# Kernel tuning notes

Hardware: AMD Instinct MI355X
Metric: run time of the kernel (lower is better)

Reference implementation:

```python
import jax, jax.numpy as jnp
import numpy as np

N_HEADS = 32
N_KV_HEADS = 8
HEAD_DIM = 64
ROPE_BASE = 10000.0


def _rope(t):
    # t: [b, s, h, d]; Llama-style rotate-half RoPE
    b, s, h, d = t.shape
    inv_freq = 1.0 / (ROPE_BASE ** (jnp.arange(0, d, 2, dtype=jnp.float32) / d))
    freqs = jnp.arange(s, dtype=jnp.float32)[:, None] * inv_freq[None, :]  # [s, d/2]
    cos = jnp.cos(freqs)[None, :, None, :].astype(t.dtype)
    sin = jnp.sin(freqs)[None, :, None, :].astype(t.dtype)
    t1, t2 = t[..., : d // 2], t[..., d // 2 :]
    return jnp.concatenate([t1 * cos - t2 * sin, t2 * cos + t1 * sin], axis=-1)


def setup_inputs() -> dict:
    key = jax.random.key(0)
    ks = jax.random.split(key, 5)
    b, s, d = 2, 2048, 2048
    dkv = d // (N_HEADS // N_KV_HEADS)
    sc = 1.0 / np.sqrt(d)
    return {
        "x": jax.random.normal(ks[0], (b, s, d), jnp.float32),
        "wq": jax.random.normal(ks[1], (d, d), jnp.float32) * sc,
        "wk": jax.random.normal(ks[2], (d, dkv), jnp.float32) * sc,
        "wv": jax.random.normal(ks[3], (d, dkv), jnp.float32) * sc,
        "wo": jax.random.normal(ks[4], (d, d), jnp.float32) * sc,
    }


def reference(x, wq, wk, wv, wo):
    b, s, d = x.shape
    g = N_HEADS // N_KV_HEADS
    q = (x @ wq).reshape(b, s, N_HEADS, HEAD_DIM)
    k = (x @ wk).reshape(b, s, N_KV_HEADS, HEAD_DIM)
    v = (x @ wv).reshape(b, s, N_KV_HEADS, HEAD_DIM)
    q = _rope(q)
    k = _rope(k)
    # GQA: repeat kv heads to match query heads
    k = jnp.repeat(k, g, axis=2)  # [b, s, N_HEADS, d_h]
    v = jnp.repeat(v, g, axis=2)
    scale = 1.0 / np.sqrt(HEAD_DIM)
    scores = jnp.einsum("bqhd,bkhd->bhqk", q, k) * scale  # [b, h, s, s]
    causal = jnp.tril(jnp.ones((s, s), dtype=bool))
    scores = jnp.where(causal[None, None], scores, jnp.finfo(scores.dtype).min)
    probs = jax.nn.softmax(scores, axis=-1)
    out = jnp.einsum("bhqk,bkhd->bqhd", probs, v).reshape(b, s, d)
    return out @ wo
```

## Files before the change

kernel.cpp:

```cpp
#include <hip/hip_runtime.h>
#include <hip/hip_bf16.h>
#include <stdint.h>

typedef __attribute__((ext_vector_type(8))) __bf16 bf16x8;
typedef __attribute__((ext_vector_type(4))) __bf16 bf16x4;
typedef __attribute__((ext_vector_type(4))) float f32x4;

#define QSCALE (0.125f * 1.44269504f)

#define GL16(src, dst) __builtin_amdgcn_global_load_lds( \
    (const __attribute__((address_space(1))) void*)(src), \
    (__attribute__((address_space(3))) void*)(dst), 16, 0, 0)

static __device__ inline unsigned pkbf(float a, float b) {
  __bf16 x = (__bf16)a, y = (__bf16)b;
  unsigned short ux = __builtin_bit_cast(unsigned short, x);
  unsigned short uy = __builtin_bit_cast(unsigned short, y);
  return ((unsigned)uy << 16) | ux;
}

static __device__ inline float ex2(float x) {
#if __has_builtin(__builtin_amdgcn_exp2f)
  return __builtin_amdgcn_exp2f(x);
#else
  float r;
  asm("v_exp_f32 %0, %1" : "=v"(r) : "v"(x));
  return r;
#endif
}

__global__ void k_cvt(const float* __restrict__ in, __bf16* __restrict__ out, int n8) {
  int i = blockIdx.x * blockDim.x + threadIdx.x;
  if (i >= n8) return;
  const float4* p = (const float4*)(in) + (size_t)i * 2;
  float4 a = p[0], b = p[1];
  bf16x8 o;
  o[0] = (__bf16)a.x; o[1] = (__bf16)a.y; o[2] = (__bf16)a.z; o[3] = (__bf16)a.w;
  o[4] = (__bf16)b.x; o[5] = (__bf16)b.y; o[6] = (__bf16)b.z; o[7] = (__bf16)b.w;
  ((bf16x8*)out)[i] = o;
}

__global__ void k_tconv(const float* __restrict__ w, __bf16* __restrict__ wT, int K, int N) {
  __shared__ float tile[32][33];
  int n0 = blockIdx.x * 32, k0 = blockIdx.y * 32;
  int tx = threadIdx.x, ty = threadIdx.y;
#pragma unroll
  for (int i = 0; i < 32; i += 8)
    tile[ty + i][tx] = w[(size_t)(k0 + ty + i) * N + n0 + tx];
  __syncthreads();
#pragma unroll
  for (int i = 0; i < 32; i += 8)
    wT[(size_t)(n0 + ty + i) * K + k0 + tx] = (__bf16)tile[tx][ty + i];
}

__global__ void k_ropetab(float* __restrict__ ct, float* __restrict__ st) {
  int i = blockIdx.x * blockDim.x + threadIdx.x;
  if (i >= 2048 * 32) return;
  int s = i >> 5, j = i & 31;
  float invf = powf(10000.0f, -(float)j / 32.0f);
  float fr = (float)s * invf;
  ct[i] = cosf(fr);
  st[i] = sinf(fr);
}

template <int BN, int NW, int WPN, int MODE>
__global__ __launch_bounds__(NW * 64, NW / 4) void k_gemm256(const __bf16* __restrict__ A,
                                                             const __bf16* __restrict__ BT,
                                                             void* __restrict__ C0,
                                                             __bf16* __restrict__ kb,
                                                             __bf16* __restrict__ vt,
                                                             const float* __restrict__ ct,
                                                             const float* __restrict__ st,
                                                             int K, int NBN) {
  constexpr int WPM = NW / WPN;
  constexpr int MF = 256 / WPM / 16;
  constexpr int NF = BN / WPN / 16;
  constexpr int MH = MF / 2;
  constexpr int CHA = 256 * 8;
  constexpr int CHB = BN * 8;
  constexpr int PA = CHA / (NW * 64);
  constexpr int RA = CHA - PA * NW * 64;
  constexpr int PB = CHB / (NW * 64);
  static_assert(CHB % (NW * 64) == 0, "B chunks must tile threads");
  static_assert(RA % 64 == 0, "A remainder must be wave-aligned");
  static_assert(NF == 4, "epilogue assumes 64-col wave window");
  constexpr int LB = PB;
  constexpr int LA0 = PA + (RA > 0 ? 1 : 0);
  constexpr int LA1 = PA;
  constexpr int NS0 = 2 * LA0 + LB, NS1 = 2 * LA1 + LB;
  constexpr int NM0 = LA0 + LB, NM1 = LA1 + LB;
  __shared__ __align__(16) __bf16 lA[3][256 * 64];
  __shared__ __align__(16) __bf16 lB[2][BN * 64];
  int bid = blockIdx.x;
  int lg = (bid & 7) * ((int)gridDim.x >> 3) + (bid >> 3);
  int bm = (lg / NBN) << 8;
  int bn = (lg % NBN) * BN;
  int tid = threadIdx.x, l = tid & 63, w = tid >> 6;
  int wr = w / WPN, wc = w % WPN;
  int lrow = l & 15, lk = l >> 4;
  int NT = K >> 6;
  f32x4 acc[MF][NF] = {};

#define STGA(T, BUF)                                                          \
  do {                                                                        \
    int k0_ = (T) << 6;                                                       \
    _Pragma("unroll") for (int i_ = 0; i_ < PA; i_++) {                       \
      int ch_ = i_ * (NW * 64) + tid;                                         \
      int r_ = ch_ >> 3, c_ = ch_ & 7;                                        \
      GL16(A + (size_t)(bm + r_) * K + k0_ + ((c_ ^ (r_ & 7)) << 3),          \
           &lA[BUF][(i_ * (NW * 64) + (w << 6)) * 8]);                        \
    }                                                                         \
    if constexpr (RA > 0) {                                                   \
      if (tid < RA) {                                                         \
        int ch_ = PA * (NW * 64) + tid;                                       \
        int r_ = ch_ >> 3, c_ = ch_ & 7;                                      \
        GL16(A + (size_t)(bm + r_) * K + k0_ + ((c_ ^ (r_ & 7)) << 3),        \
             &lA[BUF][(PA * (NW * 64) + (w << 6)) * 8]);                      \
      }                                                                       \
    }                                                                         \
  } while (0)

#define STGB(T, BUF)                                                          \
  do {                                                                        \
    int k0_ = (T) << 6;                                                       \
    _Pragma("unroll") for (int i_ = 0; i_ < PB; i_++) {                       \
      int ch_ = i_ * (NW * 64) + tid;                                         \
      int r_ = ch_ >> 3, c_ = ch_ & 7;                                        \
      GL16(BT + (size_t)(bn + r_) * K + k0_ + ((c_ ^ (r_ & 7)) << 3),         \
           &lB[BUF][(i_ * (NW * 64) + (w << 6)) * 8]);                        \
    }                                                                         \
  } while (0)

#define WAIT_STEADY()                                                         \
  do {                                                                        \
    if constexpr (RA > 0) {                                                   \
      if (w < (RA >> 6))                                                      \
        asm volatile("s_waitcnt vmcnt(%0)" ::"i"(NS0) : "memory");            \
      else                                                                    \
        asm volatile("s_waitcnt vmcnt(%0)" ::"i"(NS1) : "memory");            \
    } else {                                                                  \
      asm volatile("s_waitcnt vmcnt(%0)" ::"i"(NS1) : "memory");              \
    }                                                                         \
  } while (0)

#define WAIT_MID()                                                            \
  do {                                                                        \
    if constexpr (RA > 0) {                                                   \
      if (w < (RA >> 6))                                                      \
        asm volatile("s_waitcnt vmcnt(%0)" ::"i"(NM0) : "memory");            \
      else                                                                    \
        asm volatile("s_waitcnt vmcnt(%0)" ::"i"(NM1) : "memory");            \
    } else {                                                                  \
      asm volatile("s_waitcnt vmcnt(%0)" ::"i"(NM1) : "memory");              \
    }                                                                         \
  } while (0)

  STGB(0, 0); STGA(0, 0);
  STGB(1, 1); STGA(1, 1);
  STGA(2, 2);
  WAIT_STEADY();
  __builtin_amdgcn_sched_barrier(0);
  __builtin_amdgcn_s_barrier();

  int a0 = 0;
  for (int t = 0; t < NT; t++) {
    const char* bA = (const char*)lA[a0];
    const char* bB = (const char*)lB[t & 1];
    bf16x8 bfr[NF][2], af0[MH][2], af1[MH][2];
#pragma unroll
    for (int nf = 0; nf < NF; nf++) {
      int row = wc * (NF * 16) + nf * 16 + lrow;
#pragma unroll
      for (int kc = 0; kc < 2; kc++)
        bfr[nf][kc] = *(const bf16x8*)(bB + row * 128 +
                                       ((kc * 64 + 16 * lk) ^ ((row & 7) << 4)));
    }
#pragma unroll
    for (int mf = 0; mf < MH; mf++) {
      int row = wr * (MF * 16) + mf * 16 + lrow;
#pragma unroll
      for (int kc = 0; kc < 2; kc++)
        af0[mf][kc] = *(const bf16x8*)(bA + row * 128 +
                                       ((kc * 64 + 16 * lk) ^ ((row & 7) << 4)));
    }
#pragma unroll
    for (int mf = 0; mf < MH; mf++) {
      int row = wr * (MF * 16) + (MH + mf) * 16 + lrow;
#pragma unroll
      for (int kc = 0; kc < 2; kc++)
        af1[mf][kc] = *(const bf16x8*)(bA + row * 128 +
                                       ((kc * 64 + 16 * lk) ^ ((row & 7) << 4)));
    }
    __builtin_amdgcn_s_setprio(1);
#pragma unroll
    for (int kc = 0; kc < 2; kc++)
#pragma unroll
      for (int mf = 0; mf < MH; mf++)
#pragma unroll
        for (int nf = 0; nf < NF; nf++)
          acc[mf][nf] = __builtin_amdgcn_mfma_f32_16x16x32_bf16(af0[mf][kc], bfr[nf][kc],
                                                                acc[mf][nf], 0, 0, 0);
    __builtin_amdgcn_s_setprio(0);
    asm volatile("s_waitcnt lgkmcnt(0)" ::: "memory");
    __builtin_amdgcn_sched_barrier(0);
    __builtin_amdgcn_s_barrier();
    if (t + 2 < NT) STGB(t + 2, t & 1);
    if (t + 3 < NT) STGA(t + 3, a0);
    __builtin_amdgcn_s_setprio(1);
#pragma unroll
    for (int kc = 0; kc < 2; kc++)
#pragma unroll
      for (int mf = 0; mf < MH; mf++)
#pragma unroll
        for (int nf = 0; nf < NF; nf++)
          acc[MH + mf][nf] = __builtin_amdgcn_mfma_f32_16x16x32_bf16(
              af1[mf][kc], bfr[nf][kc], acc[MH + mf][nf], 0, 0, 0);
    __builtin_amdgcn_s_setprio(0);
    if (t + 3 < NT) {
      WAIT_STEADY();
    } else if (t + 2 < NT) {
      WAIT_MID();
    } else if (t + 1 < NT) {
      asm volatile("s_waitcnt vmcnt(0)" ::: "memory");
    }
    __builtin_amdgcn_sched_barrier(0);
    __builtin_amdgcn_s_barrier();
    a0 = (a0 == 2) ? 0 : a0 + 1;
  }
#undef STGA
#undef STGB
#undef WAIT_STEADY
#undef WAIT_MID

  if constexpr (MODE == 0) {
    int wcb = bn + wc * 64;
    __bf16* qb = (__bf16*)C0;
    if (wcb < 2048) {
#pragma unroll
      for (int mf = 0; mf < MF; mf++)
#pragma unroll
        for (int r = 0; r < 4; r++) {
          int row = bm + wr * (MF * 16) + mf * 16 + 4 * lk + r;
          int sidx = row & 2047;
#pragma unroll
          for (int nfl = 0; nfl < 2; nfl++) {
            int d = nfl * 16 + lrow;
            float c = ct[sidx * 32 + d], sn = st[sidx * 32 + d];
            float a = acc[mf][nfl][r], b2 = acc[mf][nfl + 2][r];
            qb[(size_t)row * 2048 + wcb + d] = (__bf16)((a * c - b2 * sn) * QSCALE);
            qb[(size_t)row * 2048 + wcb + d + 32] = (__bf16)((b2 * c + a * sn) * QSCALE);
          }
        }
    } else if (wcb < 2560) {
      int cb = wcb - 2048;
#pragma unroll
      for (int mf = 0; mf < MF; mf++)
#pragma unroll
        for (int r = 0; r < 4; r++) {
          int row = bm + wr * (MF * 16) + mf * 16 + 4 * lk + r;
          int sidx = row & 2047;
#pragma unroll
          for (int nfl = 0; nfl < 2; nfl++) {
            int d = nfl * 16 + lrow;
            float c = ct[sidx * 32 + d], sn = st[sidx * 32 + d];
            float a = acc[mf][nfl][r], b2 = acc[mf][nfl + 2][r];
            kb[(size_t)row * 512 + cb + d] = (__bf16)(a * c - b2 * sn);
            kb[(size_t)row * 512 + cb + d + 32] = (__bf16)(b2 * c + a * sn);
          }
        }
    } else {
      int hkk = (wcb - 2560) >> 6;
#pragma unroll
      for (int mf = 0; mf < MF; mf++)
#pragma unroll
        for (int nf = 0; nf < NF; nf++)
#pragma unroll
          for (int r = 0; r < 4; r++) {
            int row = bm + wr * (MF * 16) + mf * 16 + 4 * lk + r;
            int dd = nf * 16 + lrow;
            int bb = row >> 11, s = row & 2047;
            vt[(size_t)(((bb << 3) + hkk) * 64 + dd) * 2048 + s] = (__bf16)acc[mf][nf][r];
          }
    }
  } else {
    float* C = (float*)C0;
#pragma unroll
    for (int mf = 0; mf < MF; mf++)
#pragma unroll
      for (int nf = 0; nf < NF; nf++)
#pragma unroll
        for (int r = 0; r < 4; r++) {
          int row = bm + wr * (MF * 16) + mf * 16 + 4 * lk + r;
          int col = bn + wc * 64 + nf * 16 + lrow;
          C[(size_t)row * 2048 + col] = acc[mf][nf][r];
        }
  }
}

__global__ __launch_bounds__(256, 3) void k_attn(const __bf16* __restrict__ Q,
                                                 const __bf16* __restrict__ Kb,
                                                 const __bf16* __restrict__ VT,
                                                 __bf16* __restrict__ O) {
  __shared__ __align__(16) __bf16 lK[2][64 * 64];
  __shared__ __align__(16) __bf16 lV[2][64 * 64];
  int bid = blockIdx.x;
  int c = 63 - (bid >> 4);
  int hk = bid & 7;
  int b = (bid >> 3) & 1;
  int tid = threadIdx.x, l = tid & 63, w = tid >> 6;
  int h = hk * 4 + w;
  int lrow = l & 15, lk = l >> 4;
  int sw = (lrow & 7) << 4;
  int tl = c >> 1;

#define STAGE(BUF, T)                                                                     \
  do {                                                                                    \
    int kv0_ = (T) * 64;                                                                  \
    _Pragma("unroll") for (int i_ = 0; i_ < 2; i_++) {                                    \
      int cb_ = i_ * 256 + w * 64;                                                        \
      int chunk_ = cb_ + l;                                                               \
      int row_ = chunk_ >> 3, cc_ = chunk_ & 7;                                           \
      GL16(Kb + (size_t)(b * 2048 + kv0_ + row_) * 512 + hk * 64 +                        \
               ((cc_ ^ (row_ & 7)) << 3),                                                 \
           &lK[BUF][cb_ * 8]);                                                            \
      GL16(VT + (size_t)((b * 8 + hk) * 64 + row_) * 2048 + kv0_ +                        \
               ((cc_ ^ (row_ & 7)) << 3),                                                 \
           &lV[BUF][cb_ * 8]);                                                            \
    }                                                                                     \
  } while (0)

  bf16x8 aq[2][2];
#pragma unroll
  for (int qf = 0; qf < 2; qf++) {
    int qrow = c * 32 + qf * 16 + lrow;
    const __bf16* qp = Q + (size_t)(b * 2048 + qrow) * 2048 + h * 64 + lk * 8;
    aq[qf][0] = *(const bf16x8*)qp;
    aq[qf][1] = *(const bf16x8*)(qp + 32);
  }
  f32x4 o[2][4] = {};
  float lp[2] = {0.f, 0.f};
  STAGE(0, 0);
  for (int t = 0, buf = 0; t <= tl; t++, buf ^= 1) {
    asm volatile("s_waitcnt vmcnt(0)" ::: "memory");
    __syncthreads();
    if (t < tl) STAGE(buf ^ 1, t + 1);
    const char* K_ = (const char*)lK[buf];
    const char* V_ = (const char*)lV[buf];
    f32x4 s4[2][4];
#pragma unroll
    for (int nf = 0; nf < 4; nf++) {
      const char* kr = K_ + (nf * 16 + lrow) * 128;
      bf16x8 bk0 = *(const bf16x8*)(kr + ((16 * lk) ^ sw));
      bf16x8 bk1 = *(const bf16x8*)(kr + ((64 + 16 * lk) ^ sw));
#pragma unroll
      for (int qf = 0; qf < 2; qf++) {
        f32x4 z = {};
        z = __builtin_amdgcn_mfma_f32_16x16x32_bf16(bk0, aq[qf][0], z, 0, 0, 0);
        z = __builtin_amdgcn_mfma_f32_16x16x32_bf16(bk1, aq[qf][1], z, 0, 0, 0);
        s4[qf][nf] = z;
      }
    }
    if (t == tl) {
      int qo = (c & 1) * 32;
#pragma unroll
      for (int qf = 0; qf < 2; qf++) {
        int qoff = qo + qf * 16 + lrow;
#pragma unroll
        for (int nf = 0; nf < 4; nf++)
#pragma unroll
          for (int r = 0; r < 4; r++)
            if (nf * 16 + 4 * lk + r > qoff) s4[qf][nf][r] = -1e30f;
      }
    }
#pragma unroll
    for (int qf = 0; qf < 2; qf++) {
      float ps = 0.f;
#pragma unroll
      for (int nf = 0; nf < 4; nf++)
#pragma unroll
        for (int r = 0; r < 4; r++) {
          float pv = ex2(s4[qf][nf][r]);
          s4[qf][nf][r] = pv;
          ps += pv;
        }
      lp[qf] += ps;
    }
#pragma unroll
    for (int np = 0; np < 2; np++) {
      bf16x8 pb[2];
#pragma unroll
      for (int qf = 0; qf < 2; qf++) {
        uint4 t4;
        t4.x = pkbf(s4[qf][np][0], s4[qf][np][1]);
        t4.y = pkbf(s4[qf][np][2], s4[qf][np][3]);
        t4.z = pkbf(s4[qf][np + 2][0], s4[qf][np + 2][1]);
        t4.w = pkbf(s4[qf][np + 2][2], s4[qf][np + 2][3]);
        pb[qf] = __builtin_bit_cast(bf16x8, t4);
      }
#pragma unroll
      for (int dn = 0; dn < 4; dn++) {
        const char* vr = V_ + (dn * 16 + lrow) * 128;
        uint2 a0 = *(const uint2*)(vr + ((np * 32 + 8 * lk) ^ sw));
        uint2 a1 = *(const uint2*)(vr + (((np + 2) * 32 + 8 * lk) ^ sw));
        uint4 av;
        av.x = a0.x; av.y = a0.y; av.z = a1.x; av.w = a1.y;
        bf16x8 va = __builtin_bit_cast(bf16x8, av);
#pragma unroll
        for (int qf = 0; qf < 2; qf++)
          o[qf][dn] = __builtin_amdgcn_mfma_f32_16x16x32_bf16(va, pb[qf], o[qf][dn], 0, 0, 0);
      }
    }
  }
#pragma unroll
  for (int qf = 0; qf < 2; qf++) {
    float s = lp[qf];
    s += __shfl_xor(s, 16);
    s += __shfl_xor(s, 32);
    float inv = 1.f / s;
    int qrow = c * 32 + qf * 16 + lrow;
    __bf16* op = O + (size_t)(b * 2048 + qrow) * 2048 + h * 64 + 4 * lk;
#pragma unroll
    for (int dn = 0; dn < 4; dn++) {
      bf16x4 stv;
#pragma unroll
      for (int r = 0; r < 4; r++) stv[r] = (__bf16)(o[qf][dn][r] * inv);
      *(bf16x4*)(op + dn * 16) = stv;
    }
  }
#undef STAGE
}

extern "C" void kernel_launch(void* const* d_in, const int* in_sizes, int n_in,
                              void* d_out, int out_size, void* d_ws, size_t ws_size,
                              hipStream_t stream) {
  const float* x = (const float*)d_in[0];
  const float* wq = (const float*)d_in[1];
  const float* wk = (const float*)d_in[2];
  const float* wv = (const float*)d_in[3];
  const float* wo = (const float*)d_in[4];
  char* ws = (char*)d_ws;
  __bf16* xb    = (__bf16*)(ws + 0);
  __bf16* wqkvT = (__bf16*)(ws + 16777216);
  __bf16* woT   = (__bf16*)(ws + 29360128);
  __bf16* qb    = (__bf16*)(ws + 37748736);
  __bf16* kb    = (__bf16*)(ws + 54525952);
  __bf16* vt    = (__bf16*)(ws + 58720256);
  __bf16* ob    = (__bf16*)(ws + 62914560);
  float*  ct    = (float*)(ws + 79691776);
  float*  st    = (float*)(ws + 79953920);
  float* out = (float*)d_out;

  k_cvt<<<4096, 256, 0, stream>>>(x, xb, 1048576);
  k_tconv<<<dim3(64, 64), dim3(32, 8), 0, stream>>>(wq, wqkvT, 2048, 2048);
  k_tconv<<<dim3(16, 64), dim3(32, 8), 0, stream>>>(wk, wqkvT + (size_t)2048 * 2048, 2048, 512);
  k_tconv<<<dim3(16, 64), dim3(32, 8), 0, stream>>>(wv, wqkvT + (size_t)2560 * 2048, 2048, 512);
  k_tconv<<<dim3(64, 64), dim3(32, 8), 0, stream>>>(wo, woT, 2048, 2048);
  k_ropetab<<<256, 256, 0, stream>>>(ct, st);
  k_gemm256<192, 12, 3, 0><<<256, 768, 0, stream>>>(xb, wqkvT, qb, kb, vt, ct, st, 2048, 16);
  k_attn<<<1024, 256, 0, stream>>>(qb, kb, vt, ob);
  k_gemm256<128, 8, 2, 1><<<256, 512, 0, stream>>>(ob, woT, out, nullptr, nullptr, nullptr,
                                                   nullptr, 2048, 16);
}
```

Baseline: 168.7 us.

## Split GEMM into 2-stage variant for QKV and keep 3-stage for output projection

Rewrites k_gemm256 as a two-buffer LDS pipeline with plain blockIdx tile mapping. The QKV projection now uses it, while the previous triple-buffered kernel with the XCD-swizzled block mapping becomes k_gemm3d and is used only for the output projection. The attention kernel also raises wave priority around its MFMA sections. The two-buffer version uses less LDS, which may allow more overlap or occupancy, but it hides less load latency and drops the L2-friendly block remapping.

```diff
diff --git a/kernel.cpp b/kernel.cpp
--- a/kernel.cpp
+++ b/kernel.cpp
@@ -84,6 +84,205 @@
   static_assert(CHB % (NW * 64) == 0, "B chunks must tile threads");
   static_assert(RA % 64 == 0, "A remainder must be wave-aligned");
   static_assert(NF == 4, "epilogue assumes 64-col wave window");
+  __shared__ __align__(16) __bf16 lA[2][256 * 64];
+  __shared__ __align__(16) __bf16 lB[2][BN * 64];
+  int bm = (blockIdx.x / NBN) << 8;
+  int bn = (blockIdx.x % NBN) * BN;
+  int tid = threadIdx.x, l = tid & 63, w = tid >> 6;
+  int wr = w / WPN, wc = w % WPN;
+  int lrow = l & 15, lk = l >> 4;
+  int NT = K >> 6;
+  f32x4 acc[MF][NF] = {};
+
+#define STG(T, BUF)                                                           \
+  do {                                                                        \
+    int k0_ = (T) << 6;                                                       \
+    _Pragma("unroll") for (int i_ = 0; i_ < PA; i_++) {                       \
+      int ch_ = i_ * (NW * 64) + tid;                                         \
+      int r_ = ch_ >> 3, c_ = ch_ & 7;                                        \
+      GL16(A + (size_t)(bm + r_) * K + k0_ + ((c_ ^ (r_ & 7)) << 3),          \
+           &lA[BUF][(i_ * (NW * 64) + (w << 6)) * 8]);                        \
+    }                                                                         \
+    if constexpr (RA > 0) {                                                   \
+      if (tid < RA) {                                                         \
+        int ch_ = PA * (NW * 64) + tid;                                       \
+        int r_ = ch_ >> 3, c_ = ch_ & 7;                                      \
+        GL16(A + (size_t)(bm + r_) * K + k0_ + ((c_ ^ (r_ & 7)) << 3),        \
+             &lA[BUF][(PA * (NW * 64) + (w << 6)) * 8]);                      \
+      }                                                                       \
+    }                                                                         \
+    _Pragma("unroll") for (int i_ = 0; i_ < PB; i_++) {                       \
+      int ch_ = i_ * (NW * 64) + tid;                                         \
+      int r_ = ch_ >> 3, c_ = ch_ & 7;                                        \
+      GL16(BT + (size_t)(bn + r_) * K + k0_ + ((c_ ^ (r_ & 7)) << 3),         \
+           &lB[BUF][(i_ * (NW * 64) + (w << 6)) * 8]);                        \
+    }                                                                         \
+  } while (0)
+
+#define WAITN()                                                               \
+  do {                                                                        \
+    if constexpr (RA > 0) {                                                   \
+      if (w < (RA >> 6))                                                      \
+        asm volatile("s_waitcnt vmcnt(%0)" ::"i"(PA + PB + 1) : "memory");    \
+      else                                                                    \
+        asm volatile("s_waitcnt vmcnt(%0)" ::"i"(PA + PB) : "memory");        \
+    } else {                                                                  \
+      asm volatile("s_waitcnt vmcnt(%0)" ::"i"(PA + PB) : "memory");          \
+    }                                                                         \
+  } while (0)
+
+  STG(0, 0);
+  STG(1, 1);
+  WAITN();
+  __builtin_amdgcn_sched_barrier(0);
+  __builtin_amdgcn_s_barrier();
+
+  for (int t = 0; t < NT; t++) {
+    int buf = t & 1;
+    const char* bA = (const char*)lA[buf];
+    const char* bB = (const char*)lB[buf];
+    bf16x8 bfr[NF][2], af0[MH][2], af1[MH][2];
+#pragma unroll
+    for (int nf = 0; nf < NF; nf++) {
+      int row = wc * (NF * 16) + nf * 16 + lrow;
+#pragma unroll
+      for (int kc = 0; kc < 2; kc++)
+        bfr[nf][kc] = *(const bf16x8*)(bB + row * 128 +
+                                       ((kc * 64 + 16 * lk) ^ ((row & 7) << 4)));
+    }
+#pragma unroll
+    for (int mf = 0; mf < MH; mf++) {
+      int row = wr * (MF * 16) + mf * 16 + lrow;
+#pragma unroll
+      for (int kc = 0; kc < 2; kc++)
+        af0[mf][kc] = *(const bf16x8*)(bA + row * 128 +
+                                       ((kc * 64 + 16 * lk) ^ ((row & 7) << 4)));
+    }
+    __builtin_amdgcn_s_setprio(1);
+#pragma unroll
+    for (int kc = 0; kc < 2; kc++)
+#pragma unroll
+      for (int mf = 0; mf < MH; mf++)
+#pragma unroll
+        for (int nf = 0; nf < NF; nf++)
+          acc[mf][nf] = __builtin_amdgcn_mfma_f32_16x16x32_bf16(af0[mf][kc], bfr[nf][kc],
+                                                                acc[mf][nf], 0, 0, 0);
+    __builtin_amdgcn_s_setprio(0);
+#pragma unroll
+    for (int mf = 0; mf < MH; mf++) {
+      int row = wr * (MF * 16) + (MH + mf) * 16 + lrow;
+#pragma unroll
+      for (int kc = 0; kc < 2; kc++)
+        af1[mf][kc] = *(const bf16x8*)(bA + row * 128 +
+                                       ((kc * 64 + 16 * lk) ^ ((row & 7) << 4)));
+    }
+    asm volatile("s_waitcnt lgkmcnt(0)" ::: "memory");
+    __builtin_amdgcn_sched_barrier(0);
+    __builtin_amdgcn_s_barrier();
+    if (t + 2 < NT) STG(t + 2, buf);
+    __builtin_amdgcn_s_setprio(1);
+#pragma unroll
+    for (int kc = 0; kc < 2; kc++)
+#pragma unroll
+      for (int mf = 0; mf < MH; mf++)
+#pragma unroll
+        for (int nf = 0; nf < NF; nf++)
+          acc[MH + mf][nf] = __builtin_amdgcn_mfma_f32_16x16x32_bf16(
+              af1[mf][kc], bfr[nf][kc], acc[MH + mf][nf], 0, 0, 0);
+    __builtin_amdgcn_s_setprio(0);
+    if (t + 2 < NT) {
+      WAITN();
+    } else {
+      asm volatile("s_waitcnt vmcnt(0)" ::: "memory");
+    }
+    __builtin_amdgcn_sched_barrier(0);
+    __builtin_amdgcn_s_barrier();
+  }
+#undef STG
+#undef WAITN
+
+  if constexpr (MODE == 0) {
+    int wcb = bn + wc * 64;
+    __bf16* qb = (__bf16*)C0;
+    if (wcb < 2048) {
+#pragma unroll
+      for (int mf = 0; mf < MF; mf++)
+#pragma unroll
+        for (int r = 0; r < 4; r++) {
+          int row = bm + wr * (MF * 16) + mf * 16 + 4 * lk + r;
+          int sidx = row & 2047;
+#pragma unroll
+          for (int nfl = 0; nfl < 2; nfl++) {
+            int d = nfl * 16 + lrow;
+            float c = ct[sidx * 32 + d], sn = st[sidx * 32 + d];
+            float a = acc[mf][nfl][r], b2 = acc[mf][nfl + 2][r];
+            qb[(size_t)row * 2048 + wcb + d] = (__bf16)((a * c - b2 * sn) * QSCALE);
+            qb[(size_t)row * 2048 + wcb + d + 32] = (__bf16)((b2 * c + a * sn) * QSCALE);
+          }
+        }
+    } else if (wcb < 2560) {
+      int cb = wcb - 2048;
+#pragma unroll
+      for (int mf = 0; mf < MF; mf++)
+#pragma unroll
+        for (int r = 0; r < 4; r++) {
+          int row = bm + wr * (MF * 16) + mf * 16 + 4 * lk + r;
+          int sidx = row & 2047;
+#pragma unroll
+          for (int nfl = 0; nfl < 2; nfl++) {
+            int d = nfl * 16 + lrow;
+            float c = ct[sidx * 32 + d], sn = st[sidx * 32 + d];
+            float a = acc[mf][nfl][r], b2 = acc[mf][nfl + 2][r];
+            kb[(size_t)row * 512 + cb + d] = (__bf16)(a * c - b2 * sn);
+            kb[(size_t)row * 512 + cb + d + 32] = (__bf16)(b2 * c + a * sn);
+          }
+        }
+    } else {
+      int hkk = (wcb - 2560) >> 6;
+#pragma unroll
+      for (int mf = 0; mf < MF; mf++)
+#pragma unroll
+        for (int nf = 0; nf < NF; nf++)
+#pragma unroll
+          for (int r = 0; r < 4; r++) {
+            int row = bm + wr * (MF * 16) + mf * 16 + 4 * lk + r;
+            int dd = nf * 16 + lrow;
+            int bb = row >> 11, s = row & 2047;
+            vt[(size_t)(((bb << 3) + hkk) * 64 + dd) * 2048 + s] = (__bf16)acc[mf][nf][r];
+          }
+    }
+  } else {
+    float* C = (float*)C0;
+#pragma unroll
+    for (int mf = 0; mf < MF; mf++)
+#pragma unroll
+      for (int nf = 0; nf < NF; nf++)
+#pragma unroll
+        for (int r = 0; r < 4; r++) {
+          int row = bm + wr * (MF * 16) + mf * 16 + 4 * lk + r;
+          int col = bn + wc * 64 + nf * 16 + lrow;
+          C[(size_t)row * 2048 + col] = acc[mf][nf][r];
+        }
+  }
+}
+
+template <int BN, int NW, int WPN, int MODE>
+__global__ __launch_bounds__(NW * 64, NW / 4) void k_gemm3d(const __bf16* __restrict__ A,
+                                                            const __bf16* __restrict__ BT,
+                                                            void* __restrict__ C0,
+                                                            int K, int NBN) {
+  constexpr int WPM = NW / WPN;
+  constexpr int MF = 256 / WPM / 16;
+  constexpr int NF = BN / WPN / 16;
+  constexpr int MH = MF / 2;
+  constexpr int CHA = 256 * 8;
+  constexpr int CHB = BN * 8;
+  constexpr int PA = CHA / (NW * 64);
+  constexpr int RA = CHA - PA * NW * 64;
+  constexpr int PB = CHB / (NW * 64);
+  static_assert(CHB % (NW * 64) == 0, "B chunks must tile threads");
+  static_assert(RA % 64 == 0, "A remainder must be wave-aligned");
+  static_assert(NF == 4, "wave owns a 64-col window");
   constexpr int LB = PB;
   constexpr int LA0 = PA + (RA > 0 ? 1 : 0);
   constexpr int LA1 = PA;
@@ -232,69 +431,17 @@
 #undef WAIT_STEADY
 #undef WAIT_MID
 
-  if constexpr (MODE == 0) {
-    int wcb = bn + wc * 64;
-    __bf16* qb = (__bf16*)C0;
-    if (wcb < 2048) {
-#pragma unroll
-      for (int mf = 0; mf < MF; mf++)
-#pragma unroll
-        for (int r = 0; r < 4; r++) {
-          int row = bm + wr * (MF * 16) + mf * 16 + 4 * lk + r;
-          int sidx = row & 2047;
-#pragma unroll
-          for (int nfl = 0; nfl < 2; nfl++) {
-            int d = nfl * 16 + lrow;
-            float c = ct[sidx * 32 + d], sn = st[sidx * 32 + d];
-            float a = acc[mf][nfl][r], b2 = acc[mf][nfl + 2][r];
-            qb[(size_t)row * 2048 + wcb + d] = (__bf16)((a * c - b2 * sn) * QSCALE);
-            qb[(size_t)row * 2048 + wcb + d + 32] = (__bf16)((b2 * c + a * sn) * QSCALE);
-          }
-        }
-    } else if (wcb < 2560) {
-      int cb = wcb - 2048;
-#pragma unroll
-      for (int mf = 0; mf < MF; mf++)
-#pragma unroll
-        for (int r = 0; r < 4; r++) {
-          int row = bm + wr * (MF * 16) + mf * 16 + 4 * lk + r;
-          int sidx = row & 2047;
-#pragma unroll
-          for (int nfl = 0; nfl < 2; nfl++) {
-            int d = nfl * 16 + lrow;
-            float c = ct[sidx * 32 + d], sn = st[sidx * 32 + d];
-            float a = acc[mf][nfl][r], b2 = acc[mf][nfl + 2][r];
-            kb[(size_t)row * 512 + cb + d] = (__bf16)(a * c - b2 * sn);
-            kb[(size_t)row * 512 + cb + d + 32] = (__bf16)(b2 * c + a * sn);
-          }
-        }
-    } else {
-      int hkk = (wcb - 2560) >> 6;
-#pragma unroll
-      for (int mf = 0; mf < MF; mf++)
-#pragma unroll
-        for (int nf = 0; nf < NF; nf++)
-#pragma unroll
-          for (int r = 0; r < 4; r++) {
-            int row = bm + wr * (MF * 16) + mf * 16 + 4 * lk + r;
-            int dd = nf * 16 + lrow;
-            int bb = row >> 11, s = row & 2047;
-            vt[(size_t)(((bb << 3) + hkk) * 64 + dd) * 2048 + s] = (__bf16)acc[mf][nf][r];
-          }
-    }
-  } else {
-    float* C = (float*)C0;
-#pragma unroll
-    for (int mf = 0; mf < MF; mf++)
-#pragma unroll
-      for (int nf = 0; nf < NF; nf++)
-#pragma unroll
-        for (int r = 0; r < 4; r++) {
-          int row = bm + wr * (MF * 16) + mf * 16 + 4 * lk + r;
-          int col = bn + wc * 64 + nf * 16 + lrow;
-          C[(size_t)row * 2048 + col] = acc[mf][nf][r];
-        }
-  }
+  float* C = (float*)C0;
+#pragma unroll
+  for (int mf = 0; mf < MF; mf++)
+#pragma unroll
+    for (int nf = 0; nf < NF; nf++)
+#pragma unroll
+      for (int r = 0; r < 4; r++) {
+        int row = bm + wr * (MF * 16) + mf * 16 + 4 * lk + r;
+        int col = bn + wc * 64 + nf * 16 + lrow;
+        C[(size_t)row * 2048 + col] = acc[mf][nf][r];
+      }
 }
 
 __global__ __launch_bounds__(256, 3) void k_attn(const __bf16* __restrict__ Q,
@@ -347,6 +494,7 @@
     const char* K_ = (const char*)lK[buf];
     const char* V_ = (const char*)lV[buf];
     f32x4 s4[2][4];
+    __builtin_amdgcn_s_setprio(1);
 #pragma unroll
     for (int nf = 0; nf < 4; nf++) {
       const char* kr = K_ + (nf * 16 + lrow) * 128;
@@ -360,6 +508,7 @@
         s4[qf][nf] = z;
       }
     }
+    __builtin_amdgcn_s_setprio(0);
     if (t == tl) {
       int qo = (c & 1) * 32;
 #pragma unroll
@@ -385,6 +534,7 @@
         }
       lp[qf] += ps;
     }
+    __builtin_amdgcn_s_setprio(1);
 #pragma unroll
     for (int np = 0; np < 2; np++) {
       bf16x8 pb[2];
@@ -410,6 +560,7 @@
           o[qf][dn] = __builtin_amdgcn_mfma_f32_16x16x32_bf16(va, pb[qf], o[qf][dn], 0, 0, 0);
       }
     }
+    __builtin_amdgcn_s_setprio(0);
   }
 #pragma unroll
   for (int qf = 0; qf < 2; qf++) {
@@ -458,6 +609,5 @@
   k_ropetab<<<256, 256, 0, stream>>>(ct, st);
   k_gemm256<192, 12, 3, 0><<<256, 768, 0, stream>>>(xb, wqkvT, qb, kb, vt, ct, st, 2048, 16);
   k_attn<<<1024, 256, 0, stream>>>(qb, kb, vt, ob);
-  k_gemm256<128, 8, 2, 1><<<256, 512, 0, stream>>>(ob, woT, out, nullptr, nullptr, nullptr,
-                                                   nullptr, 2048, 16);
-}
+  k_gemm3d<128, 8, 2, 1><<<256, 512, 0, stream>>>(ob, woT, out, 2048, 16);
+}
```

Result: no change. 168.4 us (-0.2%).
